# Kernel optimization log

Hardware: AMD Instinct MI355X
Metric: run time of the kernel (lower is better)

## Reference

```python
import jax, jax.numpy as jnp
from jax import lax
import numpy as np

R_ICO = 6          # resolution exponent r
CIN, COUT = 64, 64
RIN, ROUT = 6, 6
CHARTS = 5
H, W = 2 ** R_ICO, 2 ** (R_ICO + 1)
BATCH = 4


def _build_reorder_idx(r, R):
    H_, W_ = 2 ** r, 2 ** (r + 1)
    p = 2 ** r
    idx_in = np.arange(R * 5 * H_ * W_, dtype=np.int64).reshape(R, 5, H_, W_)
    out = np.zeros((R, 5, H_ + 2, W_ + 2), dtype=np.int64)
    out[..., 1:-1, 1:-1] = idx_in
    out[..., 0, 1:p + 1] = np.roll(idx_in, 1, -3)[..., -1, p:]
    out[..., 0, p + 1:-1] = np.roll(np.roll(idx_in, 1, -3), -1, -4)[..., :, -1][..., ::-1]
    out[..., -1, 2:p + 2] = np.roll(np.roll(idx_in, -1, -3), -1, -4)[..., :, 0][..., ::-1]
    out[..., -1, p + 1:-1] = np.roll(idx_in, -1, -3)[..., 0, 0:p]
    out[..., 1:-1, 0] = np.roll(np.roll(idx_in, 1, -3), 1, -4)[..., -1, 0:p][..., ::-1]
    out[..., 2:, -1] = np.roll(np.roll(idx_in, -1, -3), 1, -4)[..., 0, p:][..., ::-1]
    return out


_REORDER = jnp.asarray(_build_reorder_idx(R_ICO, RIN))

# 'baseline' hexagonal kernel index table (idx_k2 == idx_k for baseline)
_IDX_K = np.array([
    [5, 4, -1, 6, 0, 3, -1, 1, 2],
    [4, 3, -1, 5, 0, 2, -1, 6, 1],
    [3, 2, -1, 4, 0, 1, -1, 5, 6],
    [2, 1, -1, 3, 0, 6, -1, 4, 5],
    [1, 6, -1, 2, 0, 5, -1, 3, 4],
    [6, 5, -1, 1, 0, 4, -1, 2, 3]], dtype=np.int64) % 7
# per-output-rotation roll of the Rin axis: idx_r = arange(Rin) rolled i times
_RIN_MAP = np.stack([np.roll(np.arange(RIN), i) for i in range(ROUT)])  # (Rout, Rin)
_MASK3 = np.ones((3, 3), dtype=np.float32)
_MASK3[0, 2] = 0.0  # ret[..., 0, 2] = 0
_MASK3[2, 0] = 0.0  # ret[..., 2, 0] = 0

# CleanVertices: zero the two pole vertices of each chart
_VMASK = np.ones((H, W), dtype=np.float32)
_VMASK[0, -1] = 0.0
_VMASK[-1, 0] = 0.0


def _expand_kernel(weight):
    # weight: (Cout, Cin, Rin, 7)
    # K[co, ci, i, rj, k] = weight[co, ci, rin_map[i, rj], idx_k[i, k]]
    K = weight[:, :, _RIN_MAP[:, :, None], _IDX_K[:, None, :]]  # (Cout, Cin, Rout, Rin, 9)
    K = K.transpose(0, 2, 1, 3, 4).reshape(COUT, ROUT, CIN, RIN, 3, 3)
    K = K * _MASK3  # zero hex-grid corner taps
    # kernel_type='baseline' => idx_k2 == idx_k, so 0.5*K + 0.5*K2 == K
    return K.reshape(COUT * ROUT, CIN * RIN, 3, 3)


def setup_inputs() -> dict:
    key = jax.random.key(0)
    kx, kw = jax.random.split(key)
    s = float(np.sqrt(2.0 / (3 * 3 * CIN * RIN)))
    x = jax.random.normal(kx, (BATCH, CIN, RIN, CHARTS, H, W), dtype=jnp.float32)
    weight = s * jax.random.normal(kw, (COUT, CIN, RIN, 7), dtype=jnp.float32)
    bias = jnp.zeros((COUT,), dtype=jnp.float32)
    return {"x": x, "weight": weight, "bias": bias}


def reference(x, weight, bias):
    B = x.shape[0]
    # CleanVertices on input (inside PadIco.process_vertices)
    x = x * _VMASK
    # icosahedral gather padding: [B, C, R, 5, H, W] -> [B, C, R, 5, H+2, W+2]
    xf = x.reshape(B, CIN, -1)
    xp = jnp.take(xf, _REORDER, axis=-1)
    # fold (C R) -> channels and (charts, H+2) -> height
    ximg = xp.reshape(B, CIN * RIN, CHARTS * (H + 2), W + 2)
    kernel = _expand_kernel(weight)
    y = lax.conv_general_dilated(ximg, kernel, (1, 1), ((1, 1), (1, 1)),
                                 dimension_numbers=('NCHW', 'OIHW', 'NCHW'))
    y = y + jnp.repeat(bias, ROUT)[None, :, None, None]
    y = y.reshape(B, COUT, ROUT, CHARTS, H + 2, W + 2)[..., 1:-1, 1:-1]
    # CleanVertices on output
    return y * _VMASK
```

## Files before the change

### kernel.cpp

```cpp
#include <hip/hip_runtime.h>
#include <hip/hip_bf16.h>

#define BB    4
#define CIN_  64
#define RIN_  6
#define CH_   5
#define HH    64
#define WW_   128
#define KD    384
#define MD    384
#define PH    66
#define PW    130
#define PSZ   (PH*PW)

#define NTAP 7
#define WEXP2_ELEMS (NTAP*MD*KD)
#define WEXP2_BYTES (WEXP2_ELEMS*2)
#define NBORD 388

typedef __hip_bfloat16 bf16;
typedef __attribute__((ext_vector_type(8))) short bf16x8;
typedef __attribute__((ext_vector_type(4))) float f32x4;

__device__ const int TMAP[NTAP] = {0,1,3,4,5,7,8};
__device__ const int IDXK[6][9] = {
    {5,4,6,6,0,3,6,1,2},
    {4,3,6,5,0,2,6,6,1},
    {3,2,6,4,0,1,6,5,6},
    {2,1,6,3,0,6,6,4,5},
    {1,6,6,2,0,5,6,3,4},
    {6,5,6,1,0,4,6,2,3},
};

__global__ void wexp2_kernel(const float* __restrict__ w, bf16* __restrict__ W2) {
    int e = blockIdx.x * blockDim.x + threadIdx.x;
    if (e >= WEXP2_ELEMS) return;
    int k  = e % KD;
    int m  = (e / KD) % MD;
    int tt = e / (KD * MD);
    int t  = TMAP[tt];
    int co = m / 6, ro = m % 6, ci = k / 6, ri = k % 6;
    int rw = (ri - ro + 6) % 6;
    int s  = IDXK[ro][t];
    W2[e] = __float2bfloat16(w[((co * CIN_ + ci) * RIN_ + rw) * 7 + s]);
}

__global__ __launch_bounds__(256) void pad_interior(const float* __restrict__ x,
                                                    bf16* __restrict__ P) {
    int bid  = blockIdx.x;
    int kblk = bid % 3;
    int xh   = (bid / 3) & 1;
    int y    = (bid / 6) % 64;
    int bc   = bid / 384;
    int c = bc % 5, b = bc / 5;

    int lane = threadIdx.x & 63;
    int wv   = threadIdx.x >> 6;
    int k0   = kblk * 128 + wv * 32;
    int sx   = xh * 64 + lane;
    int xx   = sx + 1;

    bool mask0 = (y == 0 && sx == 127) || (y == 63 && sx == 0);

    const float* src = x + ((((size_t)(b * 384 + k0) * 5 + c) * 64 + y) * 128 + sx);
    unsigned int hbuf[16];
    #pragma unroll
    for (int kk = 0; kk < 32; kk += 2) {
        float v1 = src[(size_t)kk * 40960];
        float v2 = src[(size_t)(kk + 1) * 40960];
        if (mask0) { v1 = 0.f; v2 = 0.f; }
        bf16 h1 = __float2bfloat16(v1);
        bf16 h2 = __float2bfloat16(v2);
        hbuf[kk >> 1] = ((unsigned int)*(unsigned short*)&h2 << 16) |
                        (unsigned int)*(unsigned short*)&h1;
    }
    bf16* dst = P + (((size_t)(b * 5 + c) * PH + (y + 1)) * PW + xx) * KD + k0;
    uint4* d4 = (uint4*)dst;
    #pragma unroll
    for (int q = 0; q < 4; ++q)
        d4[q] = make_uint4(hbuf[4*q], hbuf[4*q+1], hbuf[4*q+2], hbuf[4*q+3]);
}

__global__ void pad_border(const float* __restrict__ x, bf16* __restrict__ P) {
    int e = blockIdx.x * blockDim.x + threadIdx.x;
    if (e >= 20 * NBORD * KD) return;
    int k  = e % KD;
    int p  = (e / KD) % NBORD;
    int bc = e / (KD * NBORD);
    int c = bc % 5, b = bc / 5;
    int yy, xx;
    if (p < 130)      { yy = 0;  xx = p; }
    else if (p < 260) { yy = 65; xx = p - 130; }
    else if (p < 324) { yy = 1 + (p - 260); xx = 0; }
    else              { yy = 1 + (p - 324); xx = 129; }

    int ci = k / RIN_, r = k % RIN_;
    int sr = r, sc = c, sy = 0, sx = 0;
    bool zi = false;
    if (xx == 129) {
        if (yy >= 2) { sr = (r + 5) % 6; sc = (c + 1) % 5; sy = 0; sx = 129 - yy; }
        else zi = true;
    } else if (yy == 0) {
        if (xx >= 1 && xx <= 64)        { sc = (c + 4) % 5; sy = 63; sx = 63 + xx; }
        else if (xx >= 65 && xx <= 128) { sr = (r + 1) % 6; sc = (c + 4) % 5; sy = 128 - xx; sx = 127; }
        else zi = true;
    } else if (yy == 65) {
        if (xx >= 65 && xx <= 128)      { sc = (c + 1) % 5; sy = 0; sx = xx - 65; }
        else if (xx >= 2 && xx <= 64)   { sr = (r + 1) % 6; sc = (c + 1) % 5; sy = 65 - xx; sx = 0; }
        else zi = true;
    } else {
        sr = (r + 5) % 6; sc = (c + 4) % 5; sy = 63; sx = 64 - yy;
    }
    if (zi) { sr = 0; sc = 0; sy = 0; sx = 0; }
    float v = x[((((size_t)b * 384 + (ci * 6 + sr)) * 5 + sc) * 64 + sy) * 128 + sx];
    if ((sy == 0 && sx == 127) || (sy == 63 && sx == 0)) v = 0.f;
    P[(((size_t)(b * 5 + c) * PH + yy) * PW + xx) * KD + k] = __float2bfloat16(v);
}

#define DYP 0x2950
#define DXP 0x2644

#define GLD(g, l) __builtin_amdgcn_global_load_lds( \
    (const __attribute__((address_space(1))) void*)(g), \
    (__attribute__((address_space(3))) void*)(l), 16, 0, 0)
#define MFMA_(a, b, c) __builtin_amdgcn_mfma_f32_16x16x32_bf16((a), (b), (c), 0, 0, 0)

__global__ __launch_bounds__(256, 2) void conv_mfma4(
        const bf16* __restrict__ P, const bf16* __restrict__ W2,
        const float* __restrict__ bias, float* __restrict__ out) {
    __shared__ __align__(16) bf16 As[3][4096];
    __shared__ __align__(16) bf16 Bs[3][8192];

    const int bid = blockIdx.x;
    const int w   = (bid & 7) * 240 + (bid >> 3);
    const int mblk  = w % 3;
    const int ntile = (w / 3) % 32;
    const int bc    = w / 96;
    const int c = bc % 5, b = bc / 5;
    const int y0 = ntile * 2;

    const int tid  = threadIdx.x;
    const int lane = tid & 63;
    const int wv   = tid >> 6;
    const int lm   = lane & 15, lg = lane >> 4;

    const bf16* Pslice = P + (size_t)(b * 5 + c) * PSZ * KD;

    int oA[8], oB[4];
    #pragma unroll
    for (int i = 0; i < 8; ++i) {
        int mm = i * 16 + lm;
        oA[i] = (mm * 4 + (lg ^ ((mm >> 1) & 3))) * 16;
    }
    #pragma unroll
    for (int j = 0; j < 4; ++j) {
        int nn = wv * 64 + j * 16 + lm;
        oB[j] = (nn * 4 + (lg ^ ((nn >> 1) & 3))) * 16;
    }
    const char* Ab = (const char*)&As[0][0];
    const char* Bb = (const char*)&Bs[0][0];

    const bf16* gA[2];
    #pragma unroll
    for (int q = 0; q < 2; ++q) {
        int s = wv * 128 + q * 64 + lane;
        int row = s >> 2, j = s & 3;
        gA[q] = W2 + (size_t)(mblk * 128 + row) * KD + ((j ^ ((row >> 1) & 3)) << 3);
    }
    const bf16* gB[4];
    #pragma unroll
    for (int q = 0; q < 4; ++q) {
        int s = wv * 256 + q * 64 + lane;
        int col = s >> 2, j = s & 3;
        int ncol = (col & 127) + (col >> 7) * PW;
        gB[q] = Pslice + (size_t)ncol * KD + ((j ^ ((col >> 1) & 3)) << 3);
    }

    f32x4 acc[8][4] = {};

    #pragma unroll
    for (int t = 0; t < 2; ++t) {
        size_t offA = (size_t)t * 32;
        size_t offB = (size_t)y0 * PW * KD + t * 32;
        GLD(gA[0] + offA, &As[t][(wv * 128) * 8]);
        GLD(gA[1] + offA, &As[t][(wv * 128 + 64) * 8]);
        #pragma unroll
        for (int q = 0; q < 4; ++q)
            GLD(gB[q] + offB, &Bs[t][(wv * 256 + q * 64) * 8]);
    }
    asm volatile("s_waitcnt vmcnt(6)" ::: "memory");
    __builtin_amdgcn_s_barrier();

    #pragma unroll 1
    for (int tt = 0; tt < 7; ++tt) {
        #pragma unroll
        for (int kc = 0; kc < 12; ++kc) {
            const int rb   = kc % 3;
            const int sb   = (kc + 2) % 3;
            const int skc  = (kc + 2) % 12;
            const int stt  = tt + (kc + 2) / 12;
            const bool dostage = (stt < 7);

            bf16x8 a0 = *(const bf16x8*)(Ab + rb * 8192 + oA[0]);
            bf16x8 a1 = *(const bf16x8*)(Ab + rb * 8192 + oA[1]);
            bf16x8 a2 = *(const bf16x8*)(Ab + rb * 8192 + oA[2]);
            bf16x8 a3 = *(const bf16x8*)(Ab + rb * 8192 + oA[3]);
            bf16x8 a4 = *(const bf16x8*)(Ab + rb * 8192 + oA[4]);
            bf16x8 a5 = *(const bf16x8*)(Ab + rb * 8192 + oA[5]);
            bf16x8 a6 = *(const bf16x8*)(Ab + rb * 8192 + oA[6]);
            bf16x8 a7 = *(const bf16x8*)(Ab + rb * 8192 + oA[7]);
            bf16x8 b0 = *(const bf16x8*)(Bb + rb * 16384 + oB[0]);
            bf16x8 b1 = *(const bf16x8*)(Bb + rb * 16384 + oB[1]);

            size_t offA = 0, offB = 0;
            if (dostage) {
                const int dy = (DYP >> (2 * stt)) & 3;
                const int dx = (DXP >> (2 * stt)) & 3;
                offA = (size_t)stt * (MD * KD) + skc * 32;
                offB = ((size_t)(y0 + dy) * PW + dx) * KD + skc * 32;
                GLD(gA[0] + offA, &As[sb][(wv * 128) * 8]);
                GLD(gA[1] + offA, &As[sb][(wv * 128 + 64) * 8]);
                GLD(gB[0] + offB, &Bs[sb][(wv * 256) * 8]);
                GLD(gB[1] + offB, &Bs[sb][(wv * 256 + 64) * 8]);
            }
            __builtin_amdgcn_s_barrier();
            asm volatile("s_waitcnt lgkmcnt(0)" ::: "memory");
            __builtin_amdgcn_s_setprio(1);
            acc[0][0] = MFMA_(a0, b0, acc[0][0]);
            acc[1][0] = MFMA_(a1, b0, acc[1][0]);
            acc[2][0] = MFMA_(a2, b0, acc[2][0]);
            acc[3][0] = MFMA_(a3, b0, acc[3][0]);
            acc[4][0] = MFMA_(a4, b0, acc[4][0]);
            acc[5][0] = MFMA_(a5, b0, acc[5][0]);
            acc[6][0] = MFMA_(a6, b0, acc[6][0]);
            acc[7][0] = MFMA_(a7, b0, acc[7][0]);
            acc[0][1] = MFMA_(a0, b1, acc[0][1]);
            acc[1][1] = MFMA_(a1, b1, acc[1][1]);
            acc[2][1] = MFMA_(a2, b1, acc[2][1]);
            acc[3][1] = MFMA_(a3, b1, acc[3][1]);
            acc[4][1] = MFMA_(a4, b1, acc[4][1]);
            acc[5][1] = MFMA_(a5, b1, acc[5][1]);
            acc[6][1] = MFMA_(a6, b1, acc[6][1]);
            acc[7][1] = MFMA_(a7, b1, acc[7][1]);
            __builtin_amdgcn_s_setprio(0);
            __builtin_amdgcn_s_barrier();

            bf16x8 b2 = *(const bf16x8*)(Bb + rb * 16384 + oB[2]);
            bf16x8 b3 = *(const bf16x8*)(Bb + rb * 16384 + oB[3]);
            if (dostage) {
                GLD(gB[2] + offB, &Bs[sb][(wv * 256 + 128) * 8]);
                GLD(gB[3] + offB, &Bs[sb][(wv * 256 + 192) * 8]);
            }
            __builtin_amdgcn_s_barrier();
            asm volatile("s_waitcnt lgkmcnt(0)" ::: "memory");
            __builtin_amdgcn_s_setprio(1);
            acc[0][2] = MFMA_(a0, b2, acc[0][2]);
            acc[1][2] = MFMA_(a1, b2, acc[1][2]);
            acc[2][2] = MFMA_(a2, b2, acc[2][2]);
            acc[3][2] = MFMA_(a3, b2, acc[3][2]);
            acc[4][2] = MFMA_(a4, b2, acc[4][2]);
            acc[5][2] = MFMA_(a5, b2, acc[5][2]);
            acc[6][2] = MFMA_(a6, b2, acc[6][2]);
            acc[7][2] = MFMA_(a7, b2, acc[7][2]);
            acc[0][3] = MFMA_(a0, b3, acc[0][3]);
            acc[1][3] = MFMA_(a1, b3, acc[1][3]);
            acc[2][3] = MFMA_(a2, b3, acc[2][3]);
            acc[3][3] = MFMA_(a3, b3, acc[3][3]);
            acc[4][3] = MFMA_(a4, b3, acc[4][3]);
            acc[5][3] = MFMA_(a5, b3, acc[5][3]);
            acc[6][3] = MFMA_(a6, b3, acc[6][3]);
            acc[7][3] = MFMA_(a7, b3, acc[7][3]);
            __builtin_amdgcn_s_setprio(0);
            if (tt == 6 && kc >= 10) {
                asm volatile("s_waitcnt vmcnt(0)" ::: "memory");
            } else {
                asm volatile("s_waitcnt vmcnt(6)" ::: "memory");
            }
            __builtin_amdgcn_s_barrier();
        }
    }

    const int m0 = mblk * 128;
    const int yq = y0 + (wv >> 1);
    const int xb = (wv & 1) * 64;
    #pragma unroll
    for (int i = 0; i < 8; ++i) {
        #pragma unroll
        for (int r = 0; r < 4; ++r) {
            int m = m0 + i * 16 + lg * 4 + r;
            float bv = bias[m / 6];
            #pragma unroll
            for (int j = 0; j < 4; ++j) {
                int xq = xb + j * 16 + lm;
                float v = acc[i][j][r] + bv;
                if ((yq == 0 && xq == 127) || (yq == 63 && xq == 0)) v = 0.f;
                out[((size_t)(b * MD + m) * CH_ + c) * (HH * WW_) + yq * WW_ + xq] = v;
            }
        }
    }
}

extern "C" void kernel_launch(void* const* d_in, const int* in_sizes, int n_in,
                              void* d_out, int out_size, void* d_ws, size_t ws_size,
                              hipStream_t stream) {
    const float* x    = (const float*)d_in[0];
    const float* w    = (const float*)d_in[1];
    const float* bias = (const float*)d_in[2];
    float* out        = (float*)d_out;

    bf16* W2 = (bf16*)d_ws;
    bf16* P  = (bf16*)((char*)d_ws + WEXP2_BYTES);

    wexp2_kernel<<<(WEXP2_ELEMS + 255) / 256, 256, 0, stream>>>(w, W2);
    pad_interior<<<20 * 64 * 2 * 3, 256, 0, stream>>>(x, P);
    pad_border<<<(20 * NBORD * KD + 255) / 256, 256, 0, stream>>>(x, P);

    conv_mfma4<<<1920, 256, 0, stream>>>(P, W2, bias, out);
}
```

Measured before the change: 507.4 us.

## Enlarge conv tile to 128x512 and simplify per-k-step pipeline barriers

The block's N tile doubles from two output rows to four (512 columns), and each wave now holds an 8x8 grid of MFMA accumulators instead of 8x4. The grid shrinks to 960 blocks with one block per CU. The two half-step barrier phases and the setprio calls are collapsed into a single load-issue, 64-MFMA, wait, barrier sequence per k-chunk. This raises reuse of the weight tile and cuts barrier count, at the cost of doubled accumulator registers, larger LDS buffers, lower occupancy and possibly worse latency hiding.

```diff
diff --git a/kernel.cpp b/kernel.cpp
--- a/kernel.cpp
+++ b/kernel.cpp
@@ -125,19 +125,19 @@
     (__attribute__((address_space(3))) void*)(l), 16, 0, 0)
 #define MFMA_(a, b, c) __builtin_amdgcn_mfma_f32_16x16x32_bf16((a), (b), (c), 0, 0, 0)
 
-__global__ __launch_bounds__(256, 2) void conv_mfma4(
+__global__ __launch_bounds__(256, 1) void conv_mfma44(
         const bf16* __restrict__ P, const bf16* __restrict__ W2,
         const float* __restrict__ bias, float* __restrict__ out) {
-    __shared__ __align__(16) bf16 As[3][4096];
-    __shared__ __align__(16) bf16 Bs[3][8192];
+    __shared__ __align__(16) bf16 As[3][128 * 32];
+    __shared__ __align__(16) bf16 Bs[3][512 * 32];
 
     const int bid = blockIdx.x;
-    const int w   = (bid & 7) * 240 + (bid >> 3);
+    const int w   = (bid & 7) * 120 + (bid >> 3);
     const int mblk  = w % 3;
-    const int ntile = (w / 3) % 32;
-    const int bc    = w / 96;
+    const int ntile = (w / 3) % 16;
+    const int bc    = w / 48;
     const int c = bc % 5, b = bc / 5;
-    const int y0 = ntile * 2;
+    const int y0 = ntile * 4;
 
     const int tid  = threadIdx.x;
     const int lane = tid & 63;
@@ -146,15 +146,15 @@
 
     const bf16* Pslice = P + (size_t)(b * 5 + c) * PSZ * KD;
 
-    int oA[8], oB[4];
+    int oA[8], oB[8];
     #pragma unroll
     for (int i = 0; i < 8; ++i) {
         int mm = i * 16 + lm;
         oA[i] = (mm * 4 + (lg ^ ((mm >> 1) & 3))) * 16;
     }
     #pragma unroll
-    for (int j = 0; j < 4; ++j) {
-        int nn = wv * 64 + j * 16 + lm;
+    for (int j = 0; j < 8; ++j) {
+        int nn = wv * 128 + j * 16 + lm;
         oB[j] = (nn * 4 + (lg ^ ((nn >> 1) & 3))) * 16;
     }
     const char* Ab = (const char*)&As[0][0];
@@ -163,32 +163,33 @@
     const bf16* gA[2];
     #pragma unroll
     for (int q = 0; q < 2; ++q) {
-        int s = wv * 128 + q * 64 + lane;
+        int s = q * 256 + tid;
         int row = s >> 2, j = s & 3;
         gA[q] = W2 + (size_t)(mblk * 128 + row) * KD + ((j ^ ((row >> 1) & 3)) << 3);
     }
-    const bf16* gB[4];
-    #pragma unroll
-    for (int q = 0; q < 4; ++q) {
-        int s = wv * 256 + q * 64 + lane;
+    const bf16* gB[8];
+    #pragma unroll
+    for (int q = 0; q < 8; ++q) {
+        int s = q * 256 + tid;
         int col = s >> 2, j = s & 3;
         int ncol = (col & 127) + (col >> 7) * PW;
         gB[q] = Pslice + (size_t)ncol * KD + ((j ^ ((col >> 1) & 3)) << 3);
     }
 
-    f32x4 acc[8][4] = {};
+    f32x4 acc[8][8] = {};
 
     #pragma unroll
     for (int t = 0; t < 2; ++t) {
         size_t offA = (size_t)t * 32;
         size_t offB = (size_t)y0 * PW * KD + t * 32;
-        GLD(gA[0] + offA, &As[t][(wv * 128) * 8]);
-        GLD(gA[1] + offA, &As[t][(wv * 128 + 64) * 8]);
-        #pragma unroll
-        for (int q = 0; q < 4; ++q)
-            GLD(gB[q] + offB, &Bs[t][(wv * 256 + q * 64) * 8]);
-    }
-    asm volatile("s_waitcnt vmcnt(6)" ::: "memory");
+        #pragma unroll
+        for (int q = 0; q < 2; ++q)
+            GLD(gA[q] + offA, &As[t][(q * 256 + wv * 64) * 8]);
+        #pragma unroll
+        for (int q = 0; q < 8; ++q)
+            GLD(gB[q] + offB, &Bs[t][(q * 256 + wv * 64) * 8]);
+    }
+    asm volatile("s_waitcnt vmcnt(10)" ::: "memory");
     __builtin_amdgcn_s_barrier();
 
     #pragma unroll 1
@@ -200,6 +201,7 @@
             const int skc  = (kc + 2) % 12;
             const int stt  = tt + (kc + 2) / 12;
             const bool dostage = (stt < 7);
+            const bool drain   = (tt == 6 && kc >= 10);
 
             bf16x8 a0 = *(const bf16x8*)(Ab + rb * 8192 + oA[0]);
             bf16x8 a1 = *(const bf16x8*)(Ab + rb * 8192 + oA[1]);
@@ -209,80 +211,55 @@
             bf16x8 a5 = *(const bf16x8*)(Ab + rb * 8192 + oA[5]);
             bf16x8 a6 = *(const bf16x8*)(Ab + rb * 8192 + oA[6]);
             bf16x8 a7 = *(const bf16x8*)(Ab + rb * 8192 + oA[7]);
-            bf16x8 b0 = *(const bf16x8*)(Bb + rb * 16384 + oB[0]);
-            bf16x8 b1 = *(const bf16x8*)(Bb + rb * 16384 + oB[1]);
-
-            size_t offA = 0, offB = 0;
+            bf16x8 b0 = *(const bf16x8*)(Bb + rb * 32768 + oB[0]);
+            bf16x8 b1 = *(const bf16x8*)(Bb + rb * 32768 + oB[1]);
+            bf16x8 b2 = *(const bf16x8*)(Bb + rb * 32768 + oB[2]);
+            bf16x8 b3 = *(const bf16x8*)(Bb + rb * 32768 + oB[3]);
+            bf16x8 b4 = *(const bf16x8*)(Bb + rb * 32768 + oB[4]);
+            bf16x8 b5 = *(const bf16x8*)(Bb + rb * 32768 + oB[5]);
+            bf16x8 b6 = *(const bf16x8*)(Bb + rb * 32768 + oB[6]);
+            bf16x8 b7 = *(const bf16x8*)(Bb + rb * 32768 + oB[7]);
+
             if (dostage) {
                 const int dy = (DYP >> (2 * stt)) & 3;
                 const int dx = (DXP >> (2 * stt)) & 3;
-                offA = (size_t)stt * (MD * KD) + skc * 32;
-                offB = ((size_t)(y0 + dy) * PW + dx) * KD + skc * 32;
-                GLD(gA[0] + offA, &As[sb][(wv * 128) * 8]);
-                GLD(gA[1] + offA, &As[sb][(wv * 128 + 64) * 8]);
-                GLD(gB[0] + offB, &Bs[sb][(wv * 256) * 8]);
-                GLD(gB[1] + offB, &Bs[sb][(wv * 256 + 64) * 8]);
-            }
-            __builtin_amdgcn_s_barrier();
+                size_t offA = (size_t)stt * (MD * KD) + skc * 32;
+                size_t offB = ((size_t)(y0 + dy) * PW + dx) * KD + skc * 32;
+                #pragma unroll
+                for (int q = 0; q < 2; ++q)
+                    GLD(gA[q] + offA, &As[sb][(q * 256 + wv * 64) * 8]);
+                #pragma unroll
+                for (int q = 0; q < 8; ++q)
+                    GLD(gB[q] + offB, &Bs[sb][(q * 256 + wv * 64) * 8]);
+            }
+
+            #pragma unroll
+            for (int j = 0; j < 8; ++j) {
+                bf16x8 bj = (j == 0) ? b0 : (j == 1) ? b1 : (j == 2) ? b2 :
+                            (j == 3) ? b3 : (j == 4) ? b4 : (j == 5) ? b5 :
+                            (j == 6) ? b6 : b7;
+                acc[0][j] = MFMA_(a0, bj, acc[0][j]);
+                acc[1][j] = MFMA_(a1, bj, acc[1][j]);
+                acc[2][j] = MFMA_(a2, bj, acc[2][j]);
+                acc[3][j] = MFMA_(a3, bj, acc[3][j]);
+                acc[4][j] = MFMA_(a4, bj, acc[4][j]);
+                acc[5][j] = MFMA_(a5, bj, acc[5][j]);
+                acc[6][j] = MFMA_(a6, bj, acc[6][j]);
+                acc[7][j] = MFMA_(a7, bj, acc[7][j]);
+            }
+
             asm volatile("s_waitcnt lgkmcnt(0)" ::: "memory");
-            __builtin_amdgcn_s_setprio(1);
-            acc[0][0] = MFMA_(a0, b0, acc[0][0]);
-            acc[1][0] = MFMA_(a1, b0, acc[1][0]);
-            acc[2][0] = MFMA_(a2, b0, acc[2][0]);
-            acc[3][0] = MFMA_(a3, b0, acc[3][0]);
-            acc[4][0] = MFMA_(a4, b0, acc[4][0]);
-            acc[5][0] = MFMA_(a5, b0, acc[5][0]);
-            acc[6][0] = MFMA_(a6, b0, acc[6][0]);
-            acc[7][0] = MFMA_(a7, b0, acc[7][0]);
-            acc[0][1] = MFMA_(a0, b1, acc[0][1]);
-            acc[1][1] = MFMA_(a1, b1, acc[1][1]);
-            acc[2][1] = MFMA_(a2, b1, acc[2][1]);
-            acc[3][1] = MFMA_(a3, b1, acc[3][1]);
-            acc[4][1] = MFMA_(a4, b1, acc[4][1]);
-            acc[5][1] = MFMA_(a5, b1, acc[5][1]);
-            acc[6][1] = MFMA_(a6, b1, acc[6][1]);
-            acc[7][1] = MFMA_(a7, b1, acc[7][1]);
-            __builtin_amdgcn_s_setprio(0);
-            __builtin_amdgcn_s_barrier();
-
-            bf16x8 b2 = *(const bf16x8*)(Bb + rb * 16384 + oB[2]);
-            bf16x8 b3 = *(const bf16x8*)(Bb + rb * 16384 + oB[3]);
-            if (dostage) {
-                GLD(gB[2] + offB, &Bs[sb][(wv * 256 + 128) * 8]);
-                GLD(gB[3] + offB, &Bs[sb][(wv * 256 + 192) * 8]);
-            }
-            __builtin_amdgcn_s_barrier();
-            asm volatile("s_waitcnt lgkmcnt(0)" ::: "memory");
-            __builtin_amdgcn_s_setprio(1);
-            acc[0][2] = MFMA_(a0, b2, acc[0][2]);
-            acc[1][2] = MFMA_(a1, b2, acc[1][2]);
-            acc[2][2] = MFMA_(a2, b2, acc[2][2]);
-            acc[3][2] = MFMA_(a3, b2, acc[3][2]);
-            acc[4][2] = MFMA_(a4, b2, acc[4][2]);
-            acc[5][2] = MFMA_(a5, b2, acc[5][2]);
-            acc[6][2] = MFMA_(a6, b2, acc[6][2]);
-            acc[7][2] = MFMA_(a7, b2, acc[7][2]);
-            acc[0][3] = MFMA_(a0, b3, acc[0][3]);
-            acc[1][3] = MFMA_(a1, b3, acc[1][3]);
-            acc[2][3] = MFMA_(a2, b3, acc[2][3]);
-            acc[3][3] = MFMA_(a3, b3, acc[3][3]);
-            acc[4][3] = MFMA_(a4, b3, acc[4][3]);
-            acc[5][3] = MFMA_(a5, b3, acc[5][3]);
-            acc[6][3] = MFMA_(a6, b3, acc[6][3]);
-            acc[7][3] = MFMA_(a7, b3, acc[7][3]);
-            __builtin_amdgcn_s_setprio(0);
-            if (tt == 6 && kc >= 10) {
+            if (drain) {
                 asm volatile("s_waitcnt vmcnt(0)" ::: "memory");
             } else {
-                asm volatile("s_waitcnt vmcnt(6)" ::: "memory");
+                asm volatile("s_waitcnt vmcnt(10)" ::: "memory");
             }
             __builtin_amdgcn_s_barrier();
         }
     }
 
     const int m0 = mblk * 128;
-    const int yq = y0 + (wv >> 1);
-    const int xb = (wv & 1) * 64;
+    const int yq = y0 + wv;
     #pragma unroll
     for (int i = 0; i < 8; ++i) {
         #pragma unroll
@@ -290,8 +267,8 @@
             int m = m0 + i * 16 + lg * 4 + r;
             float bv = bias[m / 6];
             #pragma unroll
-            for (int j = 0; j < 4; ++j) {
-                int xq = xb + j * 16 + lm;
+            for (int j = 0; j < 8; ++j) {
+                int xq = j * 16 + lm;
                 float v = acc[i][j][r] + bv;
                 if ((yq == 0 && xq == 127) || (yq == 63 && xq == 0)) v = 0.f;
                 out[((size_t)(b * MD + m) * CH_ + c) * (HH * WW_) + yq * WW_ + xq] = v;
@@ -315,5 +292,5 @@
     pad_interior<<<20 * 64 * 2 * 3, 256, 0, stream>>>(x, P);
     pad_border<<<(20 * NBORD * KD + 255) / 256, 256, 0, stream>>>(x, P);
 
-    conv_mfma4<<<1920, 256, 0, stream>>>(P, W2, bias, out);
-}
+    conv_mfma44<<<960, 256, 0, stream>>>(P, W2, bias, out);
+}
```

After: 745.0 us. 46.8% more time.
